# Kernel tuning notes

Hardware: AMD Instinct MI355X
Metric: run time of the kernel (lower is better)

The kernel has to match this reference:

```python
import jax, jax.numpy as jnp
import numpy as np
from jax.scipy.special import logsumexp

EXPERT_NUM = 64
MOE_TOPK = 2

def setup_inputs() -> dict:
    key = jax.random.key(0)
    k1, k2 = jax.random.split(key)
    x = jax.random.normal(k1, (4, 4096, 4096), dtype=jnp.float32)
    # nn.Linear(input_size, expert_num).weight has shape [expert_num, input_size]
    W = jax.random.normal(k2, (EXPERT_NUM, 4096), dtype=jnp.float32) * (1.0 / np.sqrt(4096))
    return {"x": x, "W": W}

def reference(x, W):
    # logits: [B, S, E]
    logits = jnp.einsum('bsd,ed->bse', x, W)
    k = min(MOE_TOPK + 1, EXPERT_NUM)  # torch takes topk+1 then slices
    topk_logits, topk_indices = jax.lax.top_k(logits, k)
    topk_logits = topk_logits[..., :MOE_TOPK]     # [B, S, K]
    topk_indices = topk_indices[..., :MOE_TOPK]   # [B, S, K]
    # regularized=True: softmax over the top-k logits in float32
    topk_scores = jax.nn.softmax(topk_logits.astype(jnp.float32), axis=-1).astype(logits.dtype)
    # scatter into zeros; topk indices are unique so one-hot sum == scatter-set
    scores_filtered = jnp.sum(
        jax.nn.one_hot(topk_indices, EXPERT_NUM, dtype=logits.dtype) * topk_scores[..., None],
        axis=-2)  # [B, S, E]
    # router_z loss, per-token [B, S]
    log_z = logsumexp(logits, axis=-1)
    loss = log_z ** 2
    return logits, scores_filtered, loss
```

## Files before the change

kernel.cpp:

```cpp
#include <hip/hip_runtime.h>
#include <math.h>

#define TTOK 16384
#define DD   4096
#define EE   64
#define TM   32
#define BK   64
#define NCH  (DD / BK)
#define WCH  (EE * BK)

typedef __attribute__((ext_vector_type(8))) short short8;
typedef __attribute__((ext_vector_type(4))) float f32x4;

static __device__ __forceinline__ unsigned short f2bf(float f) {
    unsigned u = __float_as_uint(f);
    u += 0x7FFFu + ((u >> 16) & 1u);
    return (unsigned short)(u >> 16);
}
static __device__ __forceinline__ float bf2f(unsigned short h) {
    return __uint_as_float(((unsigned)h) << 16);
}
static __device__ __forceinline__ void cvt8(float4 a, float4 b, short8& hi, short8& lo) {
    const float v[8] = {a.x, a.y, a.z, a.w, b.x, b.y, b.z, b.w};
#pragma unroll
    for (int j = 0; j < 8; ++j) {
        const unsigned short h = f2bf(v[j]);
        hi[j] = (short)h;
        lo[j] = (short)f2bf(v[j] - bf2f(h));
    }
}

static __device__ __forceinline__ void gload16(const unsigned short* g, unsigned short* l) {
    __builtin_amdgcn_global_load_lds(
        (const __attribute__((address_space(1))) unsigned int*)g,
        (__attribute__((address_space(3))) unsigned int*)l, 16, 0, 0);
}

__global__ void w_convert(const float* __restrict__ W,
                          unsigned short* __restrict__ whi,
                          unsigned short* __restrict__ wlo) {
    const int t  = blockIdx.x * blockDim.x + threadIdx.x;
    const int r  = t >> 9;
    const int g  = t & 511;
    const int kc = g >> 3;
    const int j  = g & 7;
    const float* src = W + (size_t)r * DD + kc * BK + j * 8;
    const float4 a = *reinterpret_cast<const float4*>(src);
    const float4 b = *reinterpret_cast<const float4*>(src + 4);
    short8 h, l;
    cvt8(a, b, h, l);
    const int slot = kc * 512 + r * 8 + (j ^ (r & 7));
    *reinterpret_cast<short8*>(whi + (size_t)slot * 8) = h;
    *reinterpret_cast<short8*>(wlo + (size_t)slot * 8) = l;
}

__global__ __launch_bounds__(256, 2)
void moe_fused(const float* __restrict__ x,
               const unsigned short* __restrict__ whi,
               const unsigned short* __restrict__ wlo,
               float* __restrict__ out)
{
    __shared__ unsigned short xh[TM * 64];
    __shared__ unsigned short xl[TM * 64];
    __shared__ unsigned short whs[2 * WCH];
    __shared__ unsigned short wls[2 * WCH];
    __shared__ float lg[TM * 68];

    const int tid  = threadIdx.x;
    const int wv   = tid >> 6;
    const int lane = tid & 63;
    const int m    = lane & 15;
    const int q    = lane >> 4;
    const int tg   = wv >> 1;
    const int eh   = wv & 1;
    const int t0   = blockIdx.x * TM;

    const int sr = tid >> 3;
    const int sj = tid & 7;
    const int xo = sr * 64 + (sj ^ (sr & 7)) * 8;
    const float* gx = x + (size_t)(t0 + sr) * DD + sj * 8;

    const int ws0 = wv * 64 + lane;
    const int ws1 = 256 + ws0;

    f32x4 acc0 = (f32x4){0.f, 0.f, 0.f, 0.f};
    f32x4 acc1 = (f32x4){0.f, 0.f, 0.f, 0.f};

    gload16(whi + (size_t)ws0 * 8, whs + ws0 * 8);
    gload16(whi + (size_t)ws1 * 8, whs + ws1 * 8);
    gload16(wlo + (size_t)ws0 * 8, wls + ws0 * 8);
    gload16(wlo + (size_t)ws1 * 8, wls + ws1 * 8);
    __builtin_amdgcn_sched_barrier(0);
    float4 fx0 = *reinterpret_cast<const float4*>(gx);
    float4 fx1 = *reinterpret_cast<const float4*>(gx + 4);

    const int sa  = m & 7;
    const int ra  = (16 * tg + m) * 64;
    const int rb0 = (32 * eh + m) * 64;
    const int rb1 = (32 * eh + 16 + m) * 64;

    for (int kc = 0; kc < NCH; ++kc) {
        __builtin_amdgcn_s_barrier();
        __builtin_amdgcn_sched_barrier(0);
        if (kc + 1 < NCH) {
            const int nb = ((kc + 1) & 1) * WCH;
            const unsigned short* gh = whi + (size_t)(kc + 1) * WCH;
            const unsigned short* gl = wlo + (size_t)(kc + 1) * WCH;
            gload16(gh + (size_t)ws0 * 8, whs + nb + ws0 * 8);
            gload16(gh + (size_t)ws1 * 8, whs + nb + ws1 * 8);
            gload16(gl + (size_t)ws0 * 8, wls + nb + ws0 * 8);
            gload16(gl + (size_t)ws1 * 8, wls + nb + ws1 * 8);
        }
        __builtin_amdgcn_sched_barrier(0);

        {
            short8 h, l;
            cvt8(fx0, fx1, h, l);
            *reinterpret_cast<short8*>(xh + xo) = h;
            *reinterpret_cast<short8*>(xl + xo) = l;
        }
        if (kc + 1 < NCH) {
            const int off = (kc + 1) * BK;
            fx0 = *reinterpret_cast<const float4*>(gx + off);
            fx1 = *reinterpret_cast<const float4*>(gx + off + 4);
        }

        asm volatile("s_waitcnt lgkmcnt(0)" ::: "memory");
        __builtin_amdgcn_s_barrier();
        __builtin_amdgcn_sched_barrier(0);

        const int cb = (kc & 1) * WCH;
#pragma unroll
        for (int kss = 0; kss < 2; ++kss) {
            const int ca = ((4 * kss + q) ^ sa) * 8;
            const short8 ah  = *reinterpret_cast<const short8*>(xh + ra + ca);
            const short8 al  = *reinterpret_cast<const short8*>(xl + ra + ca);
            const short8 bh0 = *reinterpret_cast<const short8*>(whs + cb + rb0 + ca);
            const short8 bl0 = *reinterpret_cast<const short8*>(wls + cb + rb0 + ca);
            const short8 bh1 = *reinterpret_cast<const short8*>(whs + cb + rb1 + ca);
            const short8 bl1 = *reinterpret_cast<const short8*>(wls + cb + rb1 + ca);
            acc0 = __builtin_amdgcn_mfma_f32_16x16x32_bf16(ah, bh0, acc0, 0, 0, 0);
            acc0 = __builtin_amdgcn_mfma_f32_16x16x32_bf16(ah, bl0, acc0, 0, 0, 0);
            acc0 = __builtin_amdgcn_mfma_f32_16x16x32_bf16(al, bh0, acc0, 0, 0, 0);
            acc1 = __builtin_amdgcn_mfma_f32_16x16x32_bf16(ah, bh1, acc1, 0, 0, 0);
            acc1 = __builtin_amdgcn_mfma_f32_16x16x32_bf16(ah, bl1, acc1, 0, 0, 0);
            acc1 = __builtin_amdgcn_mfma_f32_16x16x32_bf16(al, bh1, acc1, 0, 0, 0);
        }
    }

    {
        float* lr = lg + (16 * tg + 4 * q) * 68 + 32 * eh + m;
#pragma unroll
        for (int i = 0; i < 4; ++i) {
            lr[i * 68]      = acc0[i];
            lr[i * 68 + 16] = acc1[i];
        }
    }
    __syncthreads();

    const int tt = tid >> 3;
    const int jj = tid & 7;
    const float* row = lg + tt * 68 + jj * 8;
    const float4 lv0 = *reinterpret_cast<const float4*>(row);
    const float4 lv1 = *reinterpret_cast<const float4*>(row + 4);
    const float r[8] = {lv0.x, lv0.y, lv0.z, lv0.w, lv1.x, lv1.y, lv1.z, lv1.w};

    float* gout = out + (size_t)(t0 + tt) * EE + jj * 8;
    *reinterpret_cast<float4*>(gout)     = lv0;
    *reinterpret_cast<float4*>(gout + 4) = lv1;

    float v1 = -INFINITY, v2 = -INFINITY;
    int   i1 = 0, i2 = 0;
#pragma unroll
    for (int c = 0; c < 8; ++c) {
        const int e = jj * 8 + c;
        const float v = r[c];
        if (v > v1)      { v2 = v1; i2 = i1; v1 = v; i1 = e; }
        else if (v > v2) { v2 = v;  i2 = e; }
    }
#pragma unroll
    for (int mk = 1; mk < 8; mk <<= 1) {
        const float ov1 = __shfl_xor(v1, mk);
        const int   oi1 = __shfl_xor(i1, mk);
        const float ov2 = __shfl_xor(v2, mk);
        const int   oi2 = __shfl_xor(i2, mk);
        const bool aw = (v1 > ov1) || (v1 == ov1 && i1 < oi1);
        const float c1v = aw ? v1 : ov1;  const int c1i = aw ? i1 : oi1;
        const float cav = aw ? v2 : ov2;  const int cai = aw ? i2 : oi2;
        const float cbv = aw ? ov1 : v1;  const int cbi = aw ? oi1 : i1;
        const bool bw = (cav > cbv) || (cav == cbv && cai < cbi);
        v1 = c1v; i1 = c1i;
        v2 = bw ? cav : cbv;
        i2 = bw ? cai : cbi;
    }

    float sm = 0.f;
#pragma unroll
    for (int c = 0; c < 8; ++c) sm += expf(r[c] - v1);
#pragma unroll
    for (int mk = 1; mk < 8; mk <<= 1) sm += __shfl_xor(sm, mk);

    const float logz = v1 + logf(sm);
    if (jj == 0) out[(size_t)2 * TTOK * EE + t0 + tt] = logz * logz;

    const float e21 = expf(v2 - v1);
    const float rr  = 1.f / (1.f + e21);
    const float sc1 = rr, sc2 = e21 * rr;
    float* sc = out + (size_t)TTOK * EE + (size_t)(t0 + tt) * EE + jj * 8;
    float vv[8];
#pragma unroll
    for (int c = 0; c < 8; ++c) {
        const int e = jj * 8 + c;
        vv[c] = (e == i1) ? sc1 : ((e == i2) ? sc2 : 0.f);
    }
    *reinterpret_cast<float4*>(sc)     = make_float4(vv[0], vv[1], vv[2], vv[3]);
    *reinterpret_cast<float4*>(sc + 4) = make_float4(vv[4], vv[5], vv[6], vv[7]);
}

extern "C" void kernel_launch(void* const* d_in, const int* in_sizes, int n_in,
                              void* d_out, int out_size, void* d_ws, size_t ws_size,
                              hipStream_t stream) {
    const float* x = (const float*)d_in[0];
    const float* W = (const float*)d_in[1];
    float* out = (float*)d_out;
    unsigned short* whi = (unsigned short*)d_ws;
    unsigned short* wlo = whi + (size_t)EE * DD;

    w_convert<<<dim3(EE * DD / 8 / 256), dim3(256), 0, stream>>>(W, whi, wlo);
    moe_fused<<<dim3(TTOK / TM), dim3(256), 0, stream>>>(x, whi, wlo, out);
}
```

Measured before the change: 383.8 us.

## Load pre-swizzled W fragments straight to registers, drop LDS staging for W

The W conversion kernel now writes bf16 hi/lo weights in exactly the per-lane MFMA fragment order. The main kernel can then load B operands directly from global memory into registers, double-buffered across chunks, instead of staging them through LDS with global_load_lds. The x stream is prefetched two chunks ahead with nontemporal loads, and the loop is unrolled by two with ping-pong register sets. This removes the W LDS traffic and shrinks the LDS footprint, at the cost of more VGPRs and redundant global or L2 reads of W by every block.

```diff
diff --git a/kernel.cpp b/kernel.cpp
--- a/kernel.cpp
+++ b/kernel.cpp
@@ -7,7 +7,6 @@
 #define TM   32
 #define BK   64
 #define NCH  (DD / BK)
-#define WCH  (EE * BK)
 
 typedef __attribute__((ext_vector_type(8))) short short8;
 typedef __attribute__((ext_vector_type(4))) float f32x4;
@@ -20,8 +19,8 @@
 static __device__ __forceinline__ float bf2f(unsigned short h) {
     return __uint_as_float(((unsigned)h) << 16);
 }
-static __device__ __forceinline__ void cvt8(float4 a, float4 b, short8& hi, short8& lo) {
-    const float v[8] = {a.x, a.y, a.z, a.w, b.x, b.y, b.z, b.w};
+static __device__ __forceinline__ void cvt8(f32x4 a, f32x4 b, short8& hi, short8& lo) {
+    const float v[8] = {a[0], a[1], a[2], a[3], b[0], b[1], b[2], b[3]};
 #pragma unroll
     for (int j = 0; j < 8; ++j) {
         const unsigned short h = f2bf(v[j]);
@@ -30,28 +29,24 @@
     }
 }
 
-static __device__ __forceinline__ void gload16(const unsigned short* g, unsigned short* l) {
-    __builtin_amdgcn_global_load_lds(
-        (const __attribute__((address_space(1))) unsigned int*)g,
-        (__attribute__((address_space(3))) unsigned int*)l, 16, 0, 0);
-}
-
 __global__ void w_convert(const float* __restrict__ W,
                           unsigned short* __restrict__ whi,
                           unsigned short* __restrict__ wlo) {
-    const int t  = blockIdx.x * blockDim.x + threadIdx.x;
-    const int r  = t >> 9;
-    const int g  = t & 511;
-    const int kc = g >> 3;
-    const int j  = g & 7;
-    const float* src = W + (size_t)r * DD + kc * BK + j * 8;
-    const float4 a = *reinterpret_cast<const float4*>(src);
-    const float4 b = *reinterpret_cast<const float4*>(src + 4);
+    const int t   = blockIdx.x * blockDim.x + threadIdx.x;
+    const int m   = t & 15;
+    const int q   = (t >> 4) & 3;
+    const int eg  = (t >> 6) & 3;
+    const int kss = (t >> 8) & 1;
+    const int kc  = t >> 9;
+    const int E   = eg * 16 + m;
+    const int k0  = kc * BK + kss * 32 + q * 8;
+    const float* src = W + (size_t)E * DD + k0;
+    const f32x4 a = *reinterpret_cast<const f32x4*>(src);
+    const f32x4 b = *reinterpret_cast<const f32x4*>(src + 4);
     short8 h, l;
     cvt8(a, b, h, l);
-    const int slot = kc * 512 + r * 8 + (j ^ (r & 7));
-    *reinterpret_cast<short8*>(whi + (size_t)slot * 8) = h;
-    *reinterpret_cast<short8*>(wlo + (size_t)slot * 8) = l;
+    *reinterpret_cast<short8*>(whi + (size_t)t * 8) = h;
+    *reinterpret_cast<short8*>(wlo + (size_t)t * 8) = l;
 }
 
 __global__ __launch_bounds__(256, 2)
@@ -62,8 +57,6 @@
 {
     __shared__ unsigned short xh[TM * 64];
     __shared__ unsigned short xl[TM * 64];
-    __shared__ unsigned short whs[2 * WCH];
-    __shared__ unsigned short wls[2 * WCH];
     __shared__ float lg[TM * 68];
 
     const int tid  = threadIdx.x;
@@ -80,73 +73,99 @@
     const int xo = sr * 64 + (sj ^ (sr & 7)) * 8;
     const float* gx = x + (size_t)(t0 + sr) * DD + sj * 8;
 
-    const int ws0 = wv * 64 + lane;
-    const int ws1 = 256 + ws0;
+    const int wb = eh * 1024 + lane * 8;
 
     f32x4 acc0 = (f32x4){0.f, 0.f, 0.f, 0.f};
     f32x4 acc1 = (f32x4){0.f, 0.f, 0.f, 0.f};
 
-    gload16(whi + (size_t)ws0 * 8, whs + ws0 * 8);
-    gload16(whi + (size_t)ws1 * 8, whs + ws1 * 8);
-    gload16(wlo + (size_t)ws0 * 8, wls + ws0 * 8);
-    gload16(wlo + (size_t)ws1 * 8, wls + ws1 * 8);
-    __builtin_amdgcn_sched_barrier(0);
-    float4 fx0 = *reinterpret_cast<const float4*>(gx);
-    float4 fx1 = *reinterpret_cast<const float4*>(gx + 4);
-
-    const int sa  = m & 7;
-    const int ra  = (16 * tg + m) * 64;
-    const int rb0 = (32 * eh + m) * 64;
-    const int rb1 = (32 * eh + 16 + m) * 64;
-
-    for (int kc = 0; kc < NCH; ++kc) {
-        __builtin_amdgcn_s_barrier();
-        __builtin_amdgcn_sched_barrier(0);
-        if (kc + 1 < NCH) {
-            const int nb = ((kc + 1) & 1) * WCH;
-            const unsigned short* gh = whi + (size_t)(kc + 1) * WCH;
-            const unsigned short* gl = wlo + (size_t)(kc + 1) * WCH;
-            gload16(gh + (size_t)ws0 * 8, whs + nb + ws0 * 8);
-            gload16(gh + (size_t)ws1 * 8, whs + nb + ws1 * 8);
-            gload16(gl + (size_t)ws0 * 8, wls + nb + ws0 * 8);
-            gload16(gl + (size_t)ws1 * 8, wls + nb + ws1 * 8);
-        }
-        __builtin_amdgcn_sched_barrier(0);
-
-        {
-            short8 h, l;
-            cvt8(fx0, fx1, h, l);
-            *reinterpret_cast<short8*>(xh + xo) = h;
-            *reinterpret_cast<short8*>(xl + xo) = l;
-        }
-        if (kc + 1 < NCH) {
-            const int off = (kc + 1) * BK;
-            fx0 = *reinterpret_cast<const float4*>(gx + off);
-            fx1 = *reinterpret_cast<const float4*>(gx + off + 4);
-        }
-
-        asm volatile("s_waitcnt lgkmcnt(0)" ::: "memory");
-        __builtin_amdgcn_s_barrier();
-        __builtin_amdgcn_sched_barrier(0);
-
-        const int cb = (kc & 1) * WCH;
-#pragma unroll
-        for (int kss = 0; kss < 2; ++kss) {
-            const int ca = ((4 * kss + q) ^ sa) * 8;
-            const short8 ah  = *reinterpret_cast<const short8*>(xh + ra + ca);
-            const short8 al  = *reinterpret_cast<const short8*>(xl + ra + ca);
-            const short8 bh0 = *reinterpret_cast<const short8*>(whs + cb + rb0 + ca);
-            const short8 bl0 = *reinterpret_cast<const short8*>(wls + cb + rb0 + ca);
-            const short8 bh1 = *reinterpret_cast<const short8*>(whs + cb + rb1 + ca);
-            const short8 bl1 = *reinterpret_cast<const short8*>(wls + cb + rb1 + ca);
-            acc0 = __builtin_amdgcn_mfma_f32_16x16x32_bf16(ah, bh0, acc0, 0, 0, 0);
-            acc0 = __builtin_amdgcn_mfma_f32_16x16x32_bf16(ah, bl0, acc0, 0, 0, 0);
-            acc0 = __builtin_amdgcn_mfma_f32_16x16x32_bf16(al, bh0, acc0, 0, 0, 0);
-            acc1 = __builtin_amdgcn_mfma_f32_16x16x32_bf16(ah, bh1, acc1, 0, 0, 0);
-            acc1 = __builtin_amdgcn_mfma_f32_16x16x32_bf16(ah, bl1, acc1, 0, 0, 0);
-            acc1 = __builtin_amdgcn_mfma_f32_16x16x32_bf16(al, bh1, acc1, 0, 0, 0);
-        }
-    }
+    short8 pA0, pA1, pA2, pA3, pA4, pA5, pA6, pA7;
+    short8 pB0, pB1, pB2, pB3, pB4, pB5, pB6, pB7;
+
+    {
+        const unsigned short* bh = whi + wb;
+        const unsigned short* bl = wlo + wb;
+        pA0 = *reinterpret_cast<const short8*>(bh);
+        pA1 = *reinterpret_cast<const short8*>(bh + 512);
+        pA2 = *reinterpret_cast<const short8*>(bh + 2048);
+        pA3 = *reinterpret_cast<const short8*>(bh + 2560);
+        pA4 = *reinterpret_cast<const short8*>(bl);
+        pA5 = *reinterpret_cast<const short8*>(bl + 512);
+        pA6 = *reinterpret_cast<const short8*>(bl + 2048);
+        pA7 = *reinterpret_cast<const short8*>(bl + 2560);
+    }
+    f32x4 fxA0 = __builtin_nontemporal_load(reinterpret_cast<const f32x4*>(gx));
+    f32x4 fxA1 = __builtin_nontemporal_load(reinterpret_cast<const f32x4*>(gx + 4));
+    f32x4 fxB0 = __builtin_nontemporal_load(reinterpret_cast<const f32x4*>(gx + BK));
+    f32x4 fxB1 = __builtin_nontemporal_load(reinterpret_cast<const f32x4*>(gx + BK + 4));
+
+    const int sa = m & 7;
+    const int ra = (16 * tg + m) * 64;
+
+#define CHUNK_BODY(KC, FX0, FX1, PC0, PC1, PC2, PC3, PC4, PC5, PC6, PC7,            \
+                         PN0, PN1, PN2, PN3, PN4, PN5, PN6, PN7)                    \
+    do {                                                                            \
+        __builtin_amdgcn_s_barrier();            \
+        __builtin_amdgcn_sched_barrier(0);                                          \
+        {                         \
+            const int kn_ = ((KC) + 1 < NCH) ? (KC) + 1 : NCH - 1;                  \
+            const unsigned short* bh_ = whi + (size_t)kn_ * 4096 + wb;              \
+            const unsigned short* bl_ = wlo + (size_t)kn_ * 4096 + wb;              \
+            PN0 = *reinterpret_cast<const short8*>(bh_);                            \
+            PN1 = *reinterpret_cast<const short8*>(bh_ + 512);                      \
+            PN2 = *reinterpret_cast<const short8*>(bh_ + 2048);                     \
+            PN3 = *reinterpret_cast<const short8*>(bh_ + 2560);                     \
+            PN4 = *reinterpret_cast<const short8*>(bl_);                            \
+            PN5 = *reinterpret_cast<const short8*>(bl_ + 512);                      \
+            PN6 = *reinterpret_cast<const short8*>(bl_ + 2048);                     \
+            PN7 = *reinterpret_cast<const short8*>(bl_ + 2560);                     \
+        }                                                                           \
+        __builtin_amdgcn_sched_barrier(0);                                          \
+        {                     \
+            short8 h_, l_;                                                          \
+            cvt8(FX0, FX1, h_, l_);                                                 \
+            *reinterpret_cast<short8*>(xh + xo) = h_;                               \
+            *reinterpret_cast<short8*>(xl + xo) = l_;                               \
+        }                                                                           \
+        {                           \
+            const int kf_ = ((KC) + 2 < NCH) ? (KC) + 2 : NCH - 1;                  \
+            FX0 = __builtin_nontemporal_load(                                       \
+                      reinterpret_cast<const f32x4*>(gx + kf_ * BK));               \
+            FX1 = __builtin_nontemporal_load(                                       \
+                      reinterpret_cast<const f32x4*>(gx + kf_ * BK + 4));           \
+        }                                                                           \
+        asm volatile("s_waitcnt lgkmcnt(0)" ::: "memory");   \
+        __builtin_amdgcn_s_barrier();                   \
+        __builtin_amdgcn_sched_barrier(0);                                          \
+        {                            \
+            const int ca0 = (q ^ sa) * 8;                                           \
+            const int ca1 = ((4 + q) ^ sa) * 8;                                     \
+            const short8 ah0 = *reinterpret_cast<const short8*>(xh + ra + ca0);     \
+            const short8 al0 = *reinterpret_cast<const short8*>(xl + ra + ca0);     \
+            const short8 ah1 = *reinterpret_cast<const short8*>(xh + ra + ca1);     \
+            const short8 al1 = *reinterpret_cast<const short8*>(xl + ra + ca1);     \
+            acc0 = __builtin_amdgcn_mfma_f32_16x16x32_bf16(ah0, PC0, acc0, 0, 0, 0);\
+            acc0 = __builtin_amdgcn_mfma_f32_16x16x32_bf16(ah0, PC4, acc0, 0, 0, 0);\
+            acc0 = __builtin_amdgcn_mfma_f32_16x16x32_bf16(al0, PC0, acc0, 0, 0, 0);\
+            acc1 = __builtin_amdgcn_mfma_f32_16x16x32_bf16(ah0, PC1, acc1, 0, 0, 0);\
+            acc1 = __builtin_amdgcn_mfma_f32_16x16x32_bf16(ah0, PC5, acc1, 0, 0, 0);\
+            acc1 = __builtin_amdgcn_mfma_f32_16x16x32_bf16(al0, PC1, acc1, 0, 0, 0);\
+            acc0 = __builtin_amdgcn_mfma_f32_16x16x32_bf16(ah1, PC2, acc0, 0, 0, 0);\
+            acc0 = __builtin_amdgcn_mfma_f32_16x16x32_bf16(ah1, PC6, acc0, 0, 0, 0);\
+            acc0 = __builtin_amdgcn_mfma_f32_16x16x32_bf16(al1, PC2, acc0, 0, 0, 0);\
+            acc1 = __builtin_amdgcn_mfma_f32_16x16x32_bf16(ah1, PC3, acc1, 0, 0, 0);\
+            acc1 = __builtin_amdgcn_mfma_f32_16x16x32_bf16(ah1, PC7, acc1, 0, 0, 0);\
+            acc1 = __builtin_amdgcn_mfma_f32_16x16x32_bf16(al1, PC3, acc1, 0, 0, 0);\
+        }                                                                           \
+    } while (0)
+
+    for (int kt = 0; kt < NCH / 2; ++kt) {
+        const int k0 = 2 * kt;
+        CHUNK_BODY(k0,     fxA0, fxA1, pA0, pA1, pA2, pA3, pA4, pA5, pA6, pA7,
+                                       pB0, pB1, pB2, pB3, pB4, pB5, pB6, pB7);
+        CHUNK_BODY(k0 + 1, fxB0, fxB1, pB0, pB1, pB2, pB3, pB4, pB5, pB6, pB7,
+                                       pA0, pA1, pA2, pA3, pA4, pA5, pA6, pA7);
+    }
+#undef CHUNK_BODY
 
     {
         float* lr = lg + (16 * tg + 4 * q) * 68 + 32 * eh + m;
@@ -161,13 +180,13 @@
     const int tt = tid >> 3;
     const int jj = tid & 7;
     const float* row = lg + tt * 68 + jj * 8;
-    const float4 lv0 = *reinterpret_cast<const float4*>(row);
-    const float4 lv1 = *reinterpret_cast<const float4*>(row + 4);
-    const float r[8] = {lv0.x, lv0.y, lv0.z, lv0.w, lv1.x, lv1.y, lv1.z, lv1.w};
+    const f32x4 lv0 = *reinterpret_cast<const f32x4*>(row);
+    const f32x4 lv1 = *reinterpret_cast<const f32x4*>(row + 4);
+    const float r[8] = {lv0[0], lv0[1], lv0[2], lv0[3], lv1[0], lv1[1], lv1[2], lv1[3]};
 
     float* gout = out + (size_t)(t0 + tt) * EE + jj * 8;
-    *reinterpret_cast<float4*>(gout)     = lv0;
-    *reinterpret_cast<float4*>(gout + 4) = lv1;
+    *reinterpret_cast<f32x4*>(gout)     = lv0;
+    *reinterpret_cast<f32x4*>(gout + 4) = lv1;
 
     float v1 = -INFINITY, v2 = -INFINITY;
     int   i1 = 0, i2 = 0;
@@ -213,8 +232,8 @@
         const int e = jj * 8 + c;
         vv[c] = (e == i1) ? sc1 : ((e == i2) ? sc2 : 0.f);
     }
-    *reinterpret_cast<float4*>(sc)     = make_float4(vv[0], vv[1], vv[2], vv[3]);
-    *reinterpret_cast<float4*>(sc + 4) = make_float4(vv[4], vv[5], vv[6], vv[7]);
+    *reinterpret_cast<f32x4*>(sc)     = (f32x4){vv[0], vv[1], vv[2], vv[3]};
+    *reinterpret_cast<f32x4*>(sc + 4) = (f32x4){vv[4], vv[5], vv[6], vv[7]};
 }
 
 extern "C" void kernel_launch(void* const* d_in, const int* in_sizes, int n_in,
```

New measurement: 377.8 us. About the same (-1.6%).
